# Performance work log

Hardware: AMD Instinct MI355X
Metric: run time of the kernel (lower is better)

The kernel has to match this reference:

```python
import jax, jax.numpy as jnp
import numpy as np
import math

B, T, D = 4, 2048, 1024
H, KD, VD = 16, 64, 64


def setup_inputs() -> dict:
    key = jax.random.key(0)
    ks = jax.random.split(key, 10)
    s = 1.0 / math.sqrt(D)
    x = jax.random.normal(ks[0], (B, T, D), dtype=jnp.float32)
    # causal mask: True above the diagonal (positions to be masked out)
    mask = jnp.triu(jnp.ones((1, T, T), dtype=bool), k=1)
    Wq = jax.random.normal(ks[1], (H * KD, D), dtype=jnp.float32) * s
    bq = jnp.zeros((H * KD,), dtype=jnp.float32)
    Wk = jax.random.normal(ks[2], (H * KD, D), dtype=jnp.float32) * s
    bk = jnp.zeros((H * KD,), dtype=jnp.float32)
    Wv = jax.random.normal(ks[3], (H * VD, D), dtype=jnp.float32) * s
    bv = jnp.zeros((H * VD,), dtype=jnp.float32)
    Wo = jax.random.normal(ks[4], (D, H * VD), dtype=jnp.float32) * (1.0 / math.sqrt(H * VD))
    bo = jnp.zeros((D,), dtype=jnp.float32)
    return {"x": x, "mask": mask, "Wq": Wq, "bq": bq, "Wk": Wk, "bk": bk,
            "Wv": Wv, "bv": bv, "Wo": Wo, "bo": bo}


def reference(x, mask, Wq, bq, Wk, bk, Wv, bv, Wo, bo):
    b, t, d = x.shape
    # projections, reshaped to (b, h, t, head_dim)
    q = (x @ Wq.T + bq).reshape(b, t, H, KD).transpose(0, 2, 1, 3)
    k = (x @ Wk.T + bk).reshape(b, t, H, KD).transpose(0, 2, 1, 3)
    v = (x @ Wv.T + bv).reshape(b, t, H, VD).transpose(0, 2, 1, 3)
    scores = jnp.einsum('bhqd,bhkd->bhqk', q, k) / jnp.sqrt(jnp.float32(KD))
    # mask [1,T,T] broadcasts over batch and heads
    scores = jnp.where(mask[:, None, :, :], -jnp.inf, scores)
    attn = jax.nn.softmax(scores, axis=-1)
    out = jnp.einsum('bhqk,bhkd->bhqd', attn, v)  # (b,h,t,vd)
    out = out.transpose(0, 2, 1, 3).reshape(b, t, H * VD)
    return out @ Wo.T + bo
```

## Files before the change

### kernel.cpp

```cpp
#include <hip/hip_runtime.h>
#include <hip/hip_bf16.h>
#include <stdint.h>

#define B_ 4
#define T_ 2048
#define D_ 1024
#define H_ 16
#define HD_ 64

typedef __attribute__((ext_vector_type(8))) short bf16x8;
typedef __attribute__((ext_vector_type(4))) float f32x4;
typedef __attribute__((ext_vector_type(16))) float f32x16;

static __device__ __forceinline__ short f2bf(float f) {
    __hip_bfloat16 h = __float2bfloat16(f);
    short s;
    __builtin_memcpy(&s, &h, sizeof(short));
    return s;
}

static __device__ __forceinline__ void gload16(const void* g, void* l) {
    __builtin_amdgcn_global_load_lds((const __attribute__((address_space(1))) uint32_t*)g,
                                     (__attribute__((address_space(3))) uint32_t*)l,
                                     16, 0, 0);
}

static __device__ __forceinline__ unsigned cvtpk(float lo, float hi) {
    unsigned r;
    asm("v_cvt_pk_bf16_f32 %0, %1, %2" : "=v"(r) : "v"(lo), "v"(hi));
    return r;
}
static __device__ __forceinline__ void pl32swap(unsigned& a, unsigned& b) {
    asm("v_permlane32_swap_b32 %0, %1" : "+v"(a), "+v"(b));
}

__global__ __launch_bounds__(256) void cast_kernel(const float* __restrict__ src,
                                                   short* __restrict__ dst, int n) {
    int i = (blockIdx.x * 256 + threadIdx.x) * 4;
    if (i < n) {
        float4 v = *reinterpret_cast<const float4*>(src + i);
        short4 o;
        o.x = f2bf(v.x); o.y = f2bf(v.y); o.z = f2bf(v.z); o.w = f2bf(v.w);
        *reinterpret_cast<short4*>(dst + i) = o;
    }
}

__global__ __launch_bounds__(256) void cast_w_kernel(const float* __restrict__ wq,
                                                     const float* __restrict__ wk,
                                                     const float* __restrict__ wv,
                                                     const float* __restrict__ wo,
                                                     short* __restrict__ wqkv,
                                                     short* __restrict__ wob) {
    int wsel = blockIdx.x >> 10;
    int blk = blockIdx.x & 1023;
    const float* src = wsel == 0 ? wq : (wsel == 1 ? wk : (wsel == 2 ? wv : wo));
    short* dst = wsel == 3 ? wob : (wqkv + (size_t)wsel * 1024 * 1024);
    int i = (blk * 256 + threadIdx.x) * 4;
    float4 v = *reinterpret_cast<const float4*>(src + i);
    short4 o;
    o.x = f2bf(v.x); o.y = f2bf(v.y); o.z = f2bf(v.z); o.w = f2bf(v.w);
    *reinterpret_cast<short4*>(dst + i) = o;
}

template <int MODE>
__global__ __launch_bounds__(256) void gemm_kernel(
        const short* __restrict__ A, const short* __restrict__ Bw,
        const float* __restrict__ b0, const float* __restrict__ b1, const float* __restrict__ b2,
        short* __restrict__ q_out, short* __restrict__ k_out, short* __restrict__ v_out,
        float* __restrict__ f_out) {
    const int K = 1024;
    const int n0 = blockIdx.x * 128;
    const int m0 = blockIdx.y * 128;
    const int tid = threadIdx.x;
    const int wid = tid >> 6, lane = tid & 63, g = lane >> 4, c = lane & 15;
    const int wr = wid >> 1, wc = wid & 1;

    __shared__ __align__(16) short As[128 * 32];
    __shared__ __align__(16) short Bs[128 * 32];

    f32x4 acc[4][4] = {};

    for (int k0 = 0; k0 < K; k0 += 32) {
        #pragma unroll
        for (int r = 0; r < 2; ++r) {
            int ci = r * 256 + tid;
            int row = ci >> 2, cc = ci & 3;
            gload16(A + (size_t)(m0 + row) * K + k0 + cc * 8, As + ci * 8);
            gload16(Bw + (size_t)(n0 + row) * K + k0 + cc * 8, Bs + ci * 8);
        }
        __syncthreads();
        bf16x8 af[4], bfr[4];
        #pragma unroll
        for (int mt = 0; mt < 4; ++mt)
            af[mt] = *reinterpret_cast<const bf16x8*>(As + (wr * 64 + mt * 16 + c) * 32 + g * 8);
        #pragma unroll
        for (int nt = 0; nt < 4; ++nt)
            bfr[nt] = *reinterpret_cast<const bf16x8*>(Bs + (wc * 64 + nt * 16 + c) * 32 + g * 8);
        #pragma unroll
        for (int mt = 0; mt < 4; ++mt) {
            #pragma unroll
            for (int nt = 0; nt < 4; ++nt)
                acc[mt][nt] = __builtin_amdgcn_mfma_f32_16x16x32_bf16(af[mt], bfr[nt], acc[mt][nt], 0, 0, 0);
        }
        __syncthreads();
    }

    #pragma unroll
    for (int mt = 0; mt < 4; ++mt) {
        #pragma unroll
        for (int nt = 0; nt < 4; ++nt) {
            int n = n0 + wc * 64 + nt * 16 + c;
            if (MODE == 0) {
                int part = n >> 10, n1 = n & 1023;
                const float* bias = part == 0 ? b0 : (part == 1 ? b1 : b2);
                short* op = part == 0 ? q_out : (part == 1 ? k_out : v_out);
                int h = n1 >> 6, d = n1 & 63;
                float bb = bias[n1];
                #pragma unroll
                for (int r = 0; r < 4; ++r) {
                    int m = m0 + wr * 64 + mt * 16 + g * 4 + r;
                    int b = m >> 11, t = m & (T_ - 1);
                    op[((size_t)(b * H_ + h) * T_ + t) * HD_ + d] = f2bf(acc[mt][nt][r] + bb);
                }
            } else {
                float bb = b0[n];
                #pragma unroll
                for (int r = 0; r < 4; ++r) {
                    int m = m0 + wr * 64 + mt * 16 + g * 4 + r;
                    f_out[(size_t)m * 1024 + n] = acc[mt][nt][r] + bb;
                }
            }
        }
    }
}

__global__ __launch_bounds__(256) void attn_kernel(const short* __restrict__ q,
                                                   const short* __restrict__ k,
                                                   const short* __restrict__ v,
                                                   short* __restrict__ o) {
    const int h = blockIdx.y, b = blockIdx.z;
    const size_t base = ((size_t)(b * H_ + h)) * T_ * HD_;
    const int tid = threadIdx.x;
    const int wid = tid >> 6, lane = tid & 63;
    const int ql = lane & 31, hi = lane >> 5;
    const int xr = (ql & 7) << 3;

    __shared__ __align__(16) short lds[16384];

    const int krr = tid >> 3, ksl = tid & 7;
    const int vkey = tid & 63, vd0b = tid >> 6;

    const int nQJ = T_ / 128;
    #pragma unroll 1
    for (int ph = 0; ph < 2; ++ph) {
        const int jj = ph == 0 ? (int)blockIdx.x : (nQJ - 1 - (int)blockIdx.x);
        const int q0b = jj * 128;
        const int q0w = q0b + wid * 32;
        const int qg = q0w + ql;
        const int nT = (q0b + 128) >> 6;

        bf16x8 qf[4];
        {
            const short* qrow = q + base + (size_t)qg * HD_ + hi * 8;
            #pragma unroll
            for (int st = 0; st < 4; ++st)
                qf[st] = *reinterpret_cast<const bf16x8*>(qrow + st * 16);
        }

        f32x16 oT0 = {}, oT1 = {};
        float m_r = -1e30f, l_r = 0.f;

        #pragma unroll
        for (int r = 0; r < 2; ++r) {
            int row = r * 32 + krr;
            gload16(k + base + (size_t)row * HD_ + ((ksl ^ (row & 7)) << 3),
                    lds + r * 2048 + tid * 8);
        }
        #pragma unroll
        for (int cc = 0; cc < 2; ++cc) {
            int vd0 = vd0b + cc * 4;
            bf16x8 vv = *reinterpret_cast<const bf16x8*>(v + base + (size_t)vkey * HD_ + vd0 * 8);
            #pragma unroll
            for (int j = 0; j < 8; ++j)
                lds[8192 + (vd0 * 8 + j) * 64 + (vkey ^ (j << 3))] = vv[j];
        }
        __syncthreads();

        int buf = 0;
        for (int t0 = 0; t0 < nT; ++t0) {
            const int kv0 = t0 * 64;
            const bool pf = (t0 + 1 < nT);
            bf16x8 vnext[2];
            if (pf) {
                #pragma unroll
                for (int r = 0; r < 2; ++r) {
                    int row = r * 32 + krr;
                    gload16(k + base + (size_t)(kv0 + 64 + row) * HD_ + ((ksl ^ (row & 7)) << 3),
                            lds + (buf ^ 1) * 4096 + r * 2048 + tid * 8);
                }
                #pragma unroll
                for (int cc = 0; cc < 2; ++cc)
                    vnext[cc] = *reinterpret_cast<const bf16x8*>(
                        v + base + (size_t)(kv0 + 64 + vkey) * HD_ + (vd0b + cc * 4) * 8);
            }

            if (kv0 <= q0w + 31) {
                const short* Kb = lds + buf * 4096;
                const short* Vb = lds + 8192 + buf * 4096;

                f32x16 s0 = {}, s1 = {};
                __builtin_amdgcn_s_setprio(1);
                #pragma unroll
                for (int st = 0; st < 4; ++st) {
                    int coff = (st * 16 + hi * 8) ^ xr;
                    bf16x8 ka0 = *reinterpret_cast<const bf16x8*>(Kb + ql * 64 + coff);
                    bf16x8 ka1 = *reinterpret_cast<const bf16x8*>(Kb + (32 + ql) * 64 + coff);
                    s0 = __builtin_amdgcn_mfma_f32_32x32x16_bf16(ka0, qf[st], s0, 0, 0, 0);
                    s1 = __builtin_amdgcn_mfma_f32_32x32x16_bf16(ka1, qf[st], s1, 0, 0, 0);
                }
                __builtin_amdgcn_s_setprio(0);

                const float SC = 0.18033688f;
                if (kv0 + 63 <= q0w) {
                    #pragma unroll
                    for (int i = 0; i < 16; ++i) { s0[i] *= SC; s1[i] *= SC; }
                } else {
                    #pragma unroll
                    for (int i = 0; i < 16; ++i) {
                        int krow = (i & 3) + 8 * (i >> 2) + 4 * hi;
                        s0[i] = (kv0 + krow > qg) ? -1e30f : s0[i] * SC;
                        s1[i] = (kv0 + 32 + krow > qg) ? -1e30f : s1[i] * SC;
                    }
                }

                float tm = s0[0];
                #pragma unroll
                for (int i = 1; i < 16; ++i) tm = fmaxf(tm, s0[i]);
                #pragma unroll
                for (int i = 0; i < 16; ++i) tm = fmaxf(tm, s1[i]);
                tm = fmaxf(tm, __shfl_xor(tm, 32, 64));
                float mn = fmaxf(m_r, tm);
                float al = exp2f(m_r - mn);
                m_r = mn;
                l_r *= al;
                #pragma unroll
                for (int i = 0; i < 16; ++i) { oT0[i] *= al; oT1[i] *= al; }
                float ts = 0.f;
                #pragma unroll
                for (int i = 0; i < 16; ++i) { s0[i] = exp2f(s0[i] - mn); ts += s0[i]; }
                #pragma unroll
                for (int i = 0; i < 16; ++i) { s1[i] = exp2f(s1[i] - mn); ts += s1[i]; }
                ts += __shfl_xor(ts, 32, 64);
                l_r += ts;

                unsigned c[16];
                #pragma unroll
                for (int i = 0; i < 8; ++i) c[i] = cvtpk(s0[2 * i], s0[2 * i + 1]);
                #pragma unroll
                for (int i = 0; i < 8; ++i) c[8 + i] = cvtpk(s1[2 * i], s1[2 * i + 1]);
                pl32swap(c[0], c[2]);   pl32swap(c[1], c[3]);
                pl32swap(c[4], c[6]);   pl32swap(c[5], c[7]);
                pl32swap(c[8], c[10]);  pl32swap(c[9], c[11]);
                pl32swap(c[12], c[14]); pl32swap(c[13], c[15]);
                union { unsigned u[4]; bf16x8 v8; } pb[4];
                #pragma unroll
                for (int ksx = 0; ksx < 4; ++ksx) {
                    #pragma unroll
                    for (int j = 0; j < 4; ++j) pb[ksx].u[j] = c[ksx * 4 + j];
                }

                __builtin_amdgcn_s_setprio(1);
                #pragma unroll
                for (int ksx = 0; ksx < 4; ++ksx) {
                    int coff = (ksx * 16 + hi * 8) ^ xr;
                    bf16x8 va0 = *reinterpret_cast<const bf16x8*>(Vb + ql * 64 + coff);
                    bf16x8 va1 = *reinterpret_cast<const bf16x8*>(Vb + (32 + ql) * 64 + coff);
                    oT0 = __builtin_amdgcn_mfma_f32_32x32x16_bf16(va0, pb[ksx].v8, oT0, 0, 0, 0);
                    oT1 = __builtin_amdgcn_mfma_f32_32x32x16_bf16(va1, pb[ksx].v8, oT1, 0, 0, 0);
                }
                __builtin_amdgcn_s_setprio(0);
            }

            if (pf) {
                #pragma unroll
                for (int cc = 0; cc < 2; ++cc) {
                    int vd0 = vd0b + cc * 4;
                    #pragma unroll
                    for (int j = 0; j < 8; ++j)
                        lds[8192 + (buf ^ 1) * 4096 + (vd0 * 8 + j) * 64 + (vkey ^ (j << 3))] = vnext[cc][j];
                }
            }
            __syncthreads();
            buf ^= 1;
        }

        float inv = 1.f / l_r;
        const int row = wid * 32 + ql;
        #pragma unroll
        for (int i = 0; i < 16; ++i) {
            int d0 = (i & 3) + 8 * (i >> 2) + 4 * hi;
            lds[8192 + row * 64 + (d0 ^ xr)] = f2bf(oT0[i] * inv);
            lds[8192 + row * 64 + ((d0 + 32) ^ xr)] = f2bf(oT1[i] * inv);
        }
        __syncthreads();
        #pragma unroll
        for (int rr = 0; rr < 4; ++rr) {
            int orow = rr * 32 + (tid >> 3);
            int sl = tid & 7;
            bf16x8 val = *reinterpret_cast<const bf16x8*>(lds + 8192 + orow * 64 + ((sl ^ (orow & 7)) << 3));
            *reinterpret_cast<bf16x8*>(o + ((size_t)(b * T_ + q0b + orow)) * D_ + h * HD_ + sl * 8) = val;
        }
        __syncthreads();
    }
}

extern "C" void kernel_launch(void* const* d_in, const int* in_sizes, int n_in,
                              void* d_out, int out_size, void* d_ws, size_t ws_size,
                              hipStream_t stream) {
    const float* x  = (const float*)d_in[0];
    const float* Wq = (const float*)d_in[2];
    const float* bq = (const float*)d_in[3];
    const float* Wk = (const float*)d_in[4];
    const float* bk = (const float*)d_in[5];
    const float* Wv = (const float*)d_in[6];
    const float* bv = (const float*)d_in[7];
    const float* Wo = (const float*)d_in[8];
    const float* bo = (const float*)d_in[9];
    float* out = (float*)d_out;

    const size_t NX = (size_t)B_ * T_ * D_;
    const size_t NW = (size_t)D_ * D_;

    short* ws   = (short*)d_ws;
    short* xb   = ws;
    short* ab   = ws;
    short* wqkv = xb + NX;
    short* wob  = wqkv + 3 * NW;
    short* qb   = wob + NW;
    short* kb   = qb + NX;
    short* vb   = kb + NX;

    cast_kernel<<<(int)(NX / 1024), 256, 0, stream>>>(x, xb, (int)NX);
    cast_w_kernel<<<4096, 256, 0, stream>>>(Wq, Wk, Wv, Wo, wqkv, wob);

    gemm_kernel<0><<<dim3(24, 64), 256, 0, stream>>>(xb, wqkv, bq, bk, bv, qb, kb, vb, nullptr);
    attn_kernel<<<dim3(T_ / 256, H_, B_), 256, 0, stream>>>(qb, kb, vb, ab);
    gemm_kernel<1><<<dim3(8, 64), 256, 0, stream>>>(ab, wob, bo, nullptr, nullptr, nullptr,
                                                    nullptr, nullptr, out);
}
```

Measured before the change: 351.1 us.

## Split long causal attention rows across two blocks with a merge kernel

Each block used to process two query tiles, paired for load balance. Now each block handles one query tile. The eight longest tiles are split into two KV halves that are computed by separate blocks, and their partial outputs plus (m, l) statistics are written to scratch space in the output buffer. A new merge kernel combines them. The softmax also gains lazy rescaling, which skips the accumulator rescale unless the max grows by more than 8, and tree reductions. The aim is better load balance and more parallelism, at the cost of an extra launch, extra traffic and bf16 rounding of the partial outputs.

Result: faster. 332.8 us (-5.2%).

```diff
diff --git a/kernel.cpp b/kernel.cpp
--- a/kernel.cpp
+++ b/kernel.cpp
@@ -17,6 +17,12 @@
     short s;
     __builtin_memcpy(&s, &h, sizeof(short));
     return s;
+}
+static __device__ __forceinline__ float bf2f(short s) {
+    unsigned u = ((unsigned)(unsigned short)s) << 16;
+    float f;
+    __builtin_memcpy(&f, &u, sizeof(float));
+    return f;
 }
 
 static __device__ __forceinline__ void gload16(const void* g, void* l) {
@@ -137,7 +143,9 @@
 __global__ __launch_bounds__(256) void attn_kernel(const short* __restrict__ q,
                                                    const short* __restrict__ k,
                                                    const short* __restrict__ v,
-                                                   short* __restrict__ o) {
+                                                   short* __restrict__ o,
+                                                   short* __restrict__ pO,
+                                                   float* __restrict__ pml) {
     const int h = blockIdx.y, b = blockIdx.z;
     const size_t base = ((size_t)(b * H_ + h)) * T_ * HD_;
     const int tid = threadIdx.x;
@@ -145,164 +153,203 @@
     const int ql = lane & 31, hi = lane >> 5;
     const int xr = (ql & 7) << 3;
 
+    const int bxx = blockIdx.x;
+    const int grp = bxx / 3, r3 = bxx - grp * 3;
+    int j, t_begin, t_end, s = 0;
+    bool partial;
+    if (r3 < 2) { partial = true;  j = 15 - grp; s = r3; t_begin = s * (j + 1); t_end = t_begin + (j + 1); }
+    else        { partial = false; j = 7 - grp;  t_begin = 0; t_end = 2 * j + 2; }
+
+    const int q0b = j * 128;
+    const int q0w = q0b + wid * 32;
+    const int qg = q0w + ql;
+
     __shared__ __align__(16) short lds[16384];
 
     const int krr = tid >> 3, ksl = tid & 7;
     const int vkey = tid & 63, vd0b = tid >> 6;
 
-    const int nQJ = T_ / 128;
-    #pragma unroll 1
-    for (int ph = 0; ph < 2; ++ph) {
-        const int jj = ph == 0 ? (int)blockIdx.x : (nQJ - 1 - (int)blockIdx.x);
-        const int q0b = jj * 128;
-        const int q0w = q0b + wid * 32;
-        const int qg = q0w + ql;
-        const int nT = (q0b + 128) >> 6;
-
-        bf16x8 qf[4];
-        {
-            const short* qrow = q + base + (size_t)qg * HD_ + hi * 8;
-            #pragma unroll
-            for (int st = 0; st < 4; ++st)
-                qf[st] = *reinterpret_cast<const bf16x8*>(qrow + st * 16);
-        }
-
-        f32x16 oT0 = {}, oT1 = {};
-        float m_r = -1e30f, l_r = 0.f;
-
+    bf16x8 qf[4];
+    {
+        const short* qrow = q + base + (size_t)qg * HD_ + hi * 8;
+        #pragma unroll
+        for (int st = 0; st < 4; ++st)
+            qf[st] = *reinterpret_cast<const bf16x8*>(qrow + st * 16);
+    }
+
+    f32x16 oT0 = {}, oT1 = {};
+    float m_r = -1e30f, l_r = 0.f;
+
+    {
+        const int kv0 = t_begin * 64;
         #pragma unroll
         for (int r = 0; r < 2; ++r) {
             int row = r * 32 + krr;
-            gload16(k + base + (size_t)row * HD_ + ((ksl ^ (row & 7)) << 3),
+            gload16(k + base + (size_t)(kv0 + row) * HD_ + ((ksl ^ (row & 7)) << 3),
                     lds + r * 2048 + tid * 8);
         }
         #pragma unroll
         for (int cc = 0; cc < 2; ++cc) {
             int vd0 = vd0b + cc * 4;
-            bf16x8 vv = *reinterpret_cast<const bf16x8*>(v + base + (size_t)vkey * HD_ + vd0 * 8);
-            #pragma unroll
-            for (int j = 0; j < 8; ++j)
-                lds[8192 + (vd0 * 8 + j) * 64 + (vkey ^ (j << 3))] = vv[j];
-        }
-        __syncthreads();
-
-        int buf = 0;
-        for (int t0 = 0; t0 < nT; ++t0) {
-            const int kv0 = t0 * 64;
-            const bool pf = (t0 + 1 < nT);
-            bf16x8 vnext[2];
-            if (pf) {
-                #pragma unroll
-                for (int r = 0; r < 2; ++r) {
-                    int row = r * 32 + krr;
-                    gload16(k + base + (size_t)(kv0 + 64 + row) * HD_ + ((ksl ^ (row & 7)) << 3),
-                            lds + (buf ^ 1) * 4096 + r * 2048 + tid * 8);
+            bf16x8 vv = *reinterpret_cast<const bf16x8*>(v + base + (size_t)(kv0 + vkey) * HD_ + vd0 * 8);
+            #pragma unroll
+            for (int jx = 0; jx < 8; ++jx)
+                lds[8192 + (vd0 * 8 + jx) * 64 + (vkey ^ (jx << 3))] = vv[jx];
+        }
+    }
+    __syncthreads();
+
+    int buf = 0;
+    for (int t0 = t_begin; t0 < t_end; ++t0) {
+        const int kv0 = t0 * 64;
+        const bool pf = (t0 + 1 < t_end);
+        bf16x8 vnext[2];
+        if (pf) {
+            #pragma unroll
+            for (int r = 0; r < 2; ++r) {
+                int row = r * 32 + krr;
+                gload16(k + base + (size_t)(kv0 + 64 + row) * HD_ + ((ksl ^ (row & 7)) << 3),
+                        lds + (buf ^ 1) * 4096 + r * 2048 + tid * 8);
+            }
+            #pragma unroll
+            for (int cc = 0; cc < 2; ++cc)
+                vnext[cc] = *reinterpret_cast<const bf16x8*>(
+                    v + base + (size_t)(kv0 + 64 + vkey) * HD_ + (vd0b + cc * 4) * 8);
+        }
+
+        if (kv0 <= q0w + 31) {
+            const short* Kb = lds + buf * 4096;
+            const short* Vb = lds + 8192 + buf * 4096;
+
+            f32x16 s0 = {}, s1 = {};
+            __builtin_amdgcn_s_setprio(1);
+            #pragma unroll
+            for (int st = 0; st < 4; ++st) {
+                int coff = (st * 16 + hi * 8) ^ xr;
+                bf16x8 ka0 = *reinterpret_cast<const bf16x8*>(Kb + ql * 64 + coff);
+                bf16x8 ka1 = *reinterpret_cast<const bf16x8*>(Kb + (32 + ql) * 64 + coff);
+                s0 = __builtin_amdgcn_mfma_f32_32x32x16_bf16(ka0, qf[st], s0, 0, 0, 0);
+                s1 = __builtin_amdgcn_mfma_f32_32x32x16_bf16(ka1, qf[st], s1, 0, 0, 0);
+            }
+            __builtin_amdgcn_s_setprio(0);
+
+            const float SC = 0.18033688f;
+            if (kv0 + 63 <= q0w) {
+                #pragma unroll
+                for (int i = 0; i < 16; ++i) { s0[i] *= SC; s1[i] *= SC; }
+            } else {
+                #pragma unroll
+                for (int i = 0; i < 16; ++i) {
+                    int krow = (i & 3) + 8 * (i >> 2) + 4 * hi;
+                    s0[i] = (kv0 + krow > qg) ? -1e30f : s0[i] * SC;
+                    s1[i] = (kv0 + 32 + krow > qg) ? -1e30f : s1[i] * SC;
                 }
-                #pragma unroll
-                for (int cc = 0; cc < 2; ++cc)
-                    vnext[cc] = *reinterpret_cast<const bf16x8*>(
-                        v + base + (size_t)(kv0 + 64 + vkey) * HD_ + (vd0b + cc * 4) * 8);
-            }
-
-            if (kv0 <= q0w + 31) {
-                const short* Kb = lds + buf * 4096;
-                const short* Vb = lds + 8192 + buf * 4096;
-
-                f32x16 s0 = {}, s1 = {};
-                __builtin_amdgcn_s_setprio(1);
-                #pragma unroll
-                for (int st = 0; st < 4; ++st) {
-                    int coff = (st * 16 + hi * 8) ^ xr;
-                    bf16x8 ka0 = *reinterpret_cast<const bf16x8*>(Kb + ql * 64 + coff);
-                    bf16x8 ka1 = *reinterpret_cast<const bf16x8*>(Kb + (32 + ql) * 64 + coff);
-                    s0 = __builtin_amdgcn_mfma_f32_32x32x16_bf16(ka0, qf[st], s0, 0, 0, 0);
-                    s1 = __builtin_amdgcn_mfma_f32_32x32x16_bf16(ka1, qf[st], s1, 0, 0, 0);
-                }
-                __builtin_amdgcn_s_setprio(0);
-
-                const float SC = 0.18033688f;
-                if (kv0 + 63 <= q0w) {
-                    #pragma unroll
-                    for (int i = 0; i < 16; ++i) { s0[i] *= SC; s1[i] *= SC; }
-                } else {
-                    #pragma unroll
-                    for (int i = 0; i < 16; ++i) {
-                        int krow = (i & 3) + 8 * (i >> 2) + 4 * hi;
-                        s0[i] = (kv0 + krow > qg) ? -1e30f : s0[i] * SC;
-                        s1[i] = (kv0 + 32 + krow > qg) ? -1e30f : s1[i] * SC;
-                    }
-                }
-
-                float tm = s0[0];
-                #pragma unroll
-                for (int i = 1; i < 16; ++i) tm = fmaxf(tm, s0[i]);
-                #pragma unroll
-                for (int i = 0; i < 16; ++i) tm = fmaxf(tm, s1[i]);
-                tm = fmaxf(tm, __shfl_xor(tm, 32, 64));
+            }
+
+            float t8[8], t4[4], t2[2], tm;
+            {
+                f32x16 mx;
+                #pragma unroll
+                for (int i = 0; i < 16; ++i) mx[i] = fmaxf(s0[i], s1[i]);
+                #pragma unroll
+                for (int i = 0; i < 8; ++i) t8[i] = fmaxf(mx[i], mx[i + 8]);
+                #pragma unroll
+                for (int i = 0; i < 4; ++i) t4[i] = fmaxf(t8[i], t8[i + 4]);
+                t2[0] = fmaxf(t4[0], t4[2]); t2[1] = fmaxf(t4[1], t4[3]);
+                tm = fmaxf(t2[0], t2[1]);
+            }
+            tm = fmaxf(tm, __shfl_xor(tm, 32, 64));
+
+            if (!__all(tm <= m_r + 8.f)) {
                 float mn = fmaxf(m_r, tm);
                 float al = exp2f(m_r - mn);
                 m_r = mn;
                 l_r *= al;
                 #pragma unroll
                 for (int i = 0; i < 16; ++i) { oT0[i] *= al; oT1[i] *= al; }
-                float ts = 0.f;
-                #pragma unroll
-                for (int i = 0; i < 16; ++i) { s0[i] = exp2f(s0[i] - mn); ts += s0[i]; }
-                #pragma unroll
-                for (int i = 0; i < 16; ++i) { s1[i] = exp2f(s1[i] - mn); ts += s1[i]; }
+            }
+
+            #pragma unroll
+            for (int i = 0; i < 16; ++i) s0[i] = exp2f(s0[i] - m_r);
+            #pragma unroll
+            for (int i = 0; i < 16; ++i) s1[i] = exp2f(s1[i] - m_r);
+
+            {
+                f32x16 sv = s0 + s1;
+                #pragma unroll
+                for (int i = 0; i < 8; ++i) t8[i] = sv[i] + sv[i + 8];
+                #pragma unroll
+                for (int i = 0; i < 4; ++i) t4[i] = t8[i] + t8[i + 4];
+                t2[0] = t4[0] + t4[2]; t2[1] = t4[1] + t4[3];
+                float ts = t2[0] + t2[1];
                 ts += __shfl_xor(ts, 32, 64);
                 l_r += ts;
-
-                unsigned c[16];
-                #pragma unroll
-                for (int i = 0; i < 8; ++i) c[i] = cvtpk(s0[2 * i], s0[2 * i + 1]);
-                #pragma unroll
-                for (int i = 0; i < 8; ++i) c[8 + i] = cvtpk(s1[2 * i], s1[2 * i + 1]);
-                pl32swap(c[0], c[2]);   pl32swap(c[1], c[3]);
-                pl32swap(c[4], c[6]);   pl32swap(c[5], c[7]);
-                pl32swap(c[8], c[10]);  pl32swap(c[9], c[11]);
-                pl32swap(c[12], c[14]); pl32swap(c[13], c[15]);
-                union { unsigned u[4]; bf16x8 v8; } pb[4];
-                #pragma unroll
-                for (int ksx = 0; ksx < 4; ++ksx) {
-                    #pragma unroll
-                    for (int j = 0; j < 4; ++j) pb[ksx].u[j] = c[ksx * 4 + j];
-                }
-
-                __builtin_amdgcn_s_setprio(1);
-                #pragma unroll
-                for (int ksx = 0; ksx < 4; ++ksx) {
-                    int coff = (ksx * 16 + hi * 8) ^ xr;
-                    bf16x8 va0 = *reinterpret_cast<const bf16x8*>(Vb + ql * 64 + coff);
-                    bf16x8 va1 = *reinterpret_cast<const bf16x8*>(Vb + (32 + ql) * 64 + coff);
-                    oT0 = __builtin_amdgcn_mfma_f32_32x32x16_bf16(va0, pb[ksx].v8, oT0, 0, 0, 0);
-                    oT1 = __builtin_amdgcn_mfma_f32_32x32x16_bf16(va1, pb[ksx].v8, oT1, 0, 0, 0);
-                }
-                __builtin_amdgcn_s_setprio(0);
-            }
-
-            if (pf) {
-                #pragma unroll
-                for (int cc = 0; cc < 2; ++cc) {
-                    int vd0 = vd0b + cc * 4;
-                    #pragma unroll
-                    for (int j = 0; j < 8; ++j)
-                        lds[8192 + (buf ^ 1) * 4096 + (vd0 * 8 + j) * 64 + (vkey ^ (j << 3))] = vnext[cc][j];
-                }
-            }
-            __syncthreads();
-            buf ^= 1;
-        }
-
-        float inv = 1.f / l_r;
-        const int row = wid * 32 + ql;
-        #pragma unroll
-        for (int i = 0; i < 16; ++i) {
-            int d0 = (i & 3) + 8 * (i >> 2) + 4 * hi;
-            lds[8192 + row * 64 + (d0 ^ xr)] = f2bf(oT0[i] * inv);
-            lds[8192 + row * 64 + ((d0 + 32) ^ xr)] = f2bf(oT1[i] * inv);
+            }
+
+            unsigned c[16];
+            #pragma unroll
+            for (int i = 0; i < 8; ++i) c[i] = cvtpk(s0[2 * i], s0[2 * i + 1]);
+            #pragma unroll
+            for (int i = 0; i < 8; ++i) c[8 + i] = cvtpk(s1[2 * i], s1[2 * i + 1]);
+            pl32swap(c[0], c[2]);   pl32swap(c[1], c[3]);
+            pl32swap(c[4], c[6]);   pl32swap(c[5], c[7]);
+            pl32swap(c[8], c[10]);  pl32swap(c[9], c[11]);
+            pl32swap(c[12], c[14]); pl32swap(c[13], c[15]);
+            union { unsigned u[4]; bf16x8 v8; } pb[4];
+            #pragma unroll
+            for (int ksx = 0; ksx < 4; ++ksx) {
+                #pragma unroll
+                for (int jx = 0; jx < 4; ++jx) pb[ksx].u[jx] = c[ksx * 4 + jx];
+            }
+
+            __builtin_amdgcn_s_setprio(1);
+            #pragma unroll
+            for (int ksx = 0; ksx < 4; ++ksx) {
+                int coff = (ksx * 16 + hi * 8) ^ xr;
+                bf16x8 va0 = *reinterpret_cast<const bf16x8*>(Vb + ql * 64 + coff);
+                bf16x8 va1 = *reinterpret_cast<const bf16x8*>(Vb + (32 + ql) * 64 + coff);
+                oT0 = __builtin_amdgcn_mfma_f32_32x32x16_bf16(va0, pb[ksx].v8, oT0, 0, 0, 0);
+                oT1 = __builtin_amdgcn_mfma_f32_32x32x16_bf16(va1, pb[ksx].v8, oT1, 0, 0, 0);
+            }
+            __builtin_amdgcn_s_setprio(0);
+        }
+
+        if (pf) {
+            #pragma unroll
+            for (int cc = 0; cc < 2; ++cc) {
+                int vd0 = vd0b + cc * 4;
+                #pragma unroll
+                for (int jx = 0; jx < 8; ++jx)
+                    lds[8192 + (buf ^ 1) * 4096 + (vd0 * 8 + jx) * 64 + (vkey ^ (jx << 3))] = vnext[cc][jx];
+            }
         }
         __syncthreads();
+        buf ^= 1;
+    }
+
+    float inv = 1.f / l_r;
+    const int row = wid * 32 + ql;
+    #pragma unroll
+    for (int i = 0; i < 16; ++i) {
+        int d0 = (i & 3) + 8 * (i >> 2) + 4 * hi;
+        lds[8192 + row * 64 + (d0 ^ xr)] = f2bf(oT0[i] * inv);
+        lds[8192 + row * 64 + ((d0 + 32) ^ xr)] = f2bf(oT1[i] * inv);
+    }
+    if (partial && hi == 0) {
+        size_t prow = ((((size_t)(b * H_ + h)) * 8 + (j - 8)) * 2 + s) * 128 + row;
+        *reinterpret_cast<float2*>(pml + prow * 2) = make_float2(m_r, l_r);
+    }
+    __syncthreads();
+    if (partial) {
+        size_t prow0 = ((((size_t)(b * H_ + h)) * 8 + (j - 8)) * 2 + s) * 128;
+        #pragma unroll
+        for (int rr = 0; rr < 4; ++rr) {
+            int orow = rr * 32 + (tid >> 3);
+            int sl = tid & 7;
+            bf16x8 val = *reinterpret_cast<const bf16x8*>(lds + 8192 + orow * 64 + ((sl ^ (orow & 7)) << 3));
+            *reinterpret_cast<bf16x8*>(pO + (prow0 + orow) * 64 + sl * 8) = val;
+        }
+    } else {
         #pragma unroll
         for (int rr = 0; rr < 4; ++rr) {
             int orow = rr * 32 + (tid >> 3);
@@ -310,8 +357,33 @@
             bf16x8 val = *reinterpret_cast<const bf16x8*>(lds + 8192 + orow * 64 + ((sl ^ (orow & 7)) << 3));
             *reinterpret_cast<bf16x8*>(o + ((size_t)(b * T_ + q0b + orow)) * D_ + h * HD_ + sl * 8) = val;
         }
-        __syncthreads();
-    }
+    }
+}
+
+__global__ __launch_bounds__(256) void merge_kernel(const short* __restrict__ pO,
+                                                    const float* __restrict__ pml,
+                                                    short* __restrict__ ab) {
+    int gid = blockIdx.x * 256 + threadIdx.x;
+    int d8 = gid & 7;
+    int r  = (gid >> 3) & 127;
+    int jj = (gid >> 10) & 7;
+    int bh = gid >> 13;
+    int b = bh >> 4, h = bh & 15;
+    size_t prow0 = (((size_t)bh * 8 + jj) * 2) * 128;
+    float m0 = pml[(prow0 + r) * 2],       l0 = pml[(prow0 + r) * 2 + 1];
+    float m1 = pml[(prow0 + 128 + r) * 2], l1 = pml[(prow0 + 128 + r) * 2 + 1];
+    float M = fmaxf(m0, m1);
+    float w0 = exp2f(m0 - M) * l0, w1 = exp2f(m1 - M) * l1;
+    float inv = 1.f / (w0 + w1);
+    w0 *= inv; w1 *= inv;
+    bf16x8 a = *reinterpret_cast<const bf16x8*>(pO + (prow0 + r) * 64 + d8 * 8);
+    bf16x8 c = *reinterpret_cast<const bf16x8*>(pO + (prow0 + 128 + r) * 64 + d8 * 8);
+    short res[8];
+    #pragma unroll
+    for (int i = 0; i < 8; ++i) res[i] = f2bf(w0 * bf2f(a[i]) + w1 * bf2f(c[i]));
+    int t = (jj + 8) * 128 + r;
+    *reinterpret_cast<bf16x8*>(ab + ((size_t)(b * T_ + t)) * D_ + h * HD_ + d8 * 8) =
+        *reinterpret_cast<const bf16x8*>(res);
 }
 
 extern "C" void kernel_launch(void* const* d_in, const int* in_sizes, int n_in,
@@ -339,12 +411,15 @@
     short* qb   = wob + NW;
     short* kb   = qb + NX;
     short* vb   = kb + NX;
+    short* pO   = (short*)d_out;
+    float* pml  = (float*)((short*)d_out + (size_t)64 * 8 * 2 * 128 * 64);
 
     cast_kernel<<<(int)(NX / 1024), 256, 0, stream>>>(x, xb, (int)NX);
     cast_w_kernel<<<4096, 256, 0, stream>>>(Wq, Wk, Wv, Wo, wqkv, wob);
 
     gemm_kernel<0><<<dim3(24, 64), 256, 0, stream>>>(xb, wqkv, bq, bk, bv, qb, kb, vb, nullptr);
-    attn_kernel<<<dim3(T_ / 256, H_, B_), 256, 0, stream>>>(qb, kb, vb, ab);
+    attn_kernel<<<dim3(24, H_, B_), 256, 0, stream>>>(qb, kb, vb, ab, pO, pml);
+    merge_kernel<<<2048, 256, 0, stream>>>(pO, pml, ab);
     gemm_kernel<1><<<dim3(8, 64), 256, 0, stream>>>(ab, wob, bo, nullptr, nullptr, nullptr,
                                                     nullptr, nullptr, out);
 }
```
